# Kernel tuning notes

Hardware: AMD Instinct MI355X
Metric: run time of the kernel (lower is better)

## Reference

```python
import jax, jax.numpy as jnp
import numpy as np

DIM = 1024
HEADS = 16
HEAD_DIM = DIM // HEADS


def apply_rope(x):
    # x: (B, S, H, D)
    B, S, H, D = x.shape
    half = D // 2
    freqs = 1.0 / (10000.0 ** (jnp.arange(half, dtype=jnp.float32) / half))
    pos = jnp.arange(S, dtype=jnp.float32)
    angles = pos[:, None] * freqs[None, :]          # (S, half)
    sin = jnp.sin(angles)[None, :, None, :]
    cos = jnp.cos(angles)[None, :, None, :]
    x1, x2 = x[..., :half], x[..., half:]
    return jnp.concatenate([x1 * cos - x2 * sin, x1 * sin + x2 * cos], axis=-1)


def setup_inputs() -> dict:
    key = jax.random.key(0)
    ks = jax.random.split(key, 5)
    x = jax.random.normal(ks[0], (2, 2048, DIM), dtype=jnp.float32)
    s = 1.0 / np.sqrt(DIM)
    qkv_w = jax.random.uniform(ks[1], (3 * DIM, DIM), minval=-s, maxval=s, dtype=jnp.float32)
    qkv_b = jax.random.uniform(ks[2], (3 * DIM,), minval=-s, maxval=s, dtype=jnp.float32)
    proj_w = jax.random.uniform(ks[3], (DIM, DIM), minval=-s, maxval=s, dtype=jnp.float32)
    proj_b = jax.random.uniform(ks[4], (DIM,), minval=-s, maxval=s, dtype=jnp.float32)
    return {"x": x, "qkv_w": qkv_w, "qkv_b": qkv_b, "proj_w": proj_w, "proj_b": proj_b}


def reference(x, qkv_w, qkv_b, proj_w, proj_b):
    B, S, D = x.shape
    qkv = x @ qkv_w.T + qkv_b                       # (B, S, 3D)
    q, k, v = jnp.split(qkv, 3, axis=-1)
    q = q.reshape(B, S, HEADS, HEAD_DIM)
    k = k.reshape(B, S, HEADS, HEAD_DIM)
    v = v.reshape(B, S, HEADS, HEAD_DIM)
    q = apply_rope(q)
    k = apply_rope(k)
    scale = 1.0 / np.sqrt(HEAD_DIM)
    attn = jnp.einsum('bqhd,bkhd->bhqk', q, k) * scale
    mask = jnp.triu(jnp.ones((S, S), dtype=bool), k=1)
    attn = jnp.where(mask[None, None], -1e9, attn)
    attn = jax.nn.softmax(attn, axis=-1)
    out = jnp.einsum('bhqk,bkhd->bqhd', attn, v).reshape(B, S, D)
    return out @ proj_w.T + proj_b
```

## Files before the change

kernel.cpp:

```cpp
#include <hip/hip_runtime.h>
#include <hip/hip_bf16.h>
#include <stdint.h>

typedef unsigned short u16;
typedef __attribute__((ext_vector_type(8))) short bf16x8;
typedef __attribute__((ext_vector_type(4))) float f32x4;
typedef __attribute__((ext_vector_type(16))) float f32x16;

typedef __attribute__((address_space(1))) const void gas_t;
typedef __attribute__((address_space(3))) void las_t;

#define DEV __device__ __forceinline__

DEV float bf2f(u16 v){ union{uint32_t u; float f;} x; x.u = ((uint32_t)v)<<16; return x.f; }
DEV u16 f2bf(float f){ union{float f; uint32_t u;} x; x.f=f; uint32_t r = x.u + 0x7fff + ((x.u>>16)&1u); return (u16)(r>>16); }

DEV uint32_t pk2(float a, float b){
  return (uint32_t)f2bf(a) | ((uint32_t)f2bf(b)<<16);
}

DEV uint32_t cvtpk(float a, float b){
  uint32_t r;
  asm("v_cvt_pk_bf16_f32 %0, %1, %2" : "=v"(r) : "v"(a), "v"(b));
  return r;
}

DEV void xswap(uint32_t a, uint32_t b, int hi, uint32_t& ra, uint32_t& rb){
#if __has_builtin(__builtin_amdgcn_permlane32_swap)
  auto r = __builtin_amdgcn_permlane32_swap((int)a, (int)b, false, false);
  ra = (uint32_t)r[0]; rb = (uint32_t)r[1];
#else
  uint32_t sa = (uint32_t)__shfl_xor((int)a, 32);
  uint32_t sb = (uint32_t)__shfl_xor((int)b, 32);
  ra = hi ? sb : a;
  rb = hi ? b  : sa;
#endif
}

DEV void gload_lds16(const u16* g, u16* l){
  __builtin_amdgcn_global_load_lds((gas_t*)g, (las_t*)l, 16, 0, 0);
}

__global__ void cvt_f32_bf16(const float* __restrict__ src, u16* __restrict__ dst, int n4){
  int i = blockIdx.x*blockDim.x + threadIdx.x;
  if(i < n4){
    float4 v = ((const float4*)src)[i];
    ushort4 o; o.x=f2bf(v.x); o.y=f2bf(v.y); o.z=f2bf(v.z); o.w=f2bf(v.w);
    ((ushort4*)dst)[i] = o;
  }
}

template<int OUT_F32>
__global__ __launch_bounds__(256,3)
void gemm_bt(const u16* __restrict__ A, const u16* __restrict__ Bw,
             const float* __restrict__ bias, void* __restrict__ Cp, int N)
{
  constexpr int BK = 32, KSTEPS = 1024/BK;
  __shared__ __align__(16) u16 As[3][128][BK];
  __shared__ __align__(16) u16 Bs[3][128][BK];
  const int tid = threadIdx.x, w = tid>>6, l = tid&63;
  const int a = l&15, g = l>>4;
  const int m0 = blockIdx.y*128, n0 = blockIdx.x*128;
  const int wr = w>>1, wc = w&1;
  f32x4 zero = {0.f,0.f,0.f,0.f};
  f32x4 acc[4][4];
  #pragma unroll
  for(int m=0;m<4;m++) for(int n=0;n<4;n++) acc[m][n]=zero;

  const int srow = l>>2, scol = (l&3)*8;
  const u16* Ag = A  + (size_t)(m0 + w*32 + srow)*1024 + scol;
  const u16* Bg = Bw + (size_t)(n0 + w*32 + srow)*1024 + scol;

#define STAGE(KIDX, BUF) {                                        \
    u16* ab = &As[BUF][w*32][0];                                  \
    u16* bb = &Bs[BUF][w*32][0];                                  \
    gload_lds16(Ag + (KIDX)*BK,           ab);                    \
    gload_lds16(Ag + (KIDX)*BK + 16*1024, ab + 16*BK);            \
    gload_lds16(Bg + (KIDX)*BK,           bb);                    \
    gload_lds16(Bg + (KIDX)*BK + 16*1024, bb + 16*BK);            \
  }

  STAGE(0, 0);
  STAGE(1, 1);

  int bc = 0, bn = 2;
  for(int kt=0; kt<KSTEPS; ++kt){
    if(kt+1 < KSTEPS) asm volatile("s_waitcnt vmcnt(4)" ::: "memory");
    else              asm volatile("s_waitcnt vmcnt(0)" ::: "memory");
    __builtin_amdgcn_s_barrier();
    __builtin_amdgcn_sched_barrier(0);

    if(kt+2 < KSTEPS) STAGE(kt+2, bn);

    const u16* AsB = &As[bc][0][0];
    const u16* BsB = &Bs[bc][0][0];
    bf16x8 af[4], bf[4];
    #pragma unroll
    for(int m=0;m<4;m++) af[m] = *(const bf16x8*)(AsB + (wr*64 + m*16 + a)*BK + g*8);
    #pragma unroll
    for(int n=0;n<4;n++) bf[n] = *(const bf16x8*)(BsB + (wc*64 + n*16 + a)*BK + g*8);
    #pragma unroll
    for(int m=0;m<4;m++)
      #pragma unroll
      for(int n=0;n<4;n++)
        acc[m][n] = __builtin_amdgcn_mfma_f32_16x16x32_bf16(af[m], bf[n], acc[m][n], 0,0,0);

    bc = (bc==2) ? 0 : bc+1;
    bn = (bn==2) ? 0 : bn+1;
  }
#undef STAGE

  #pragma unroll
  for(int n=0;n<4;n++){
    int col = n0 + wc*64 + n*16 + a;
    float bv = bias[col];
    #pragma unroll
    for(int m=0;m<4;m++){
      int row = m0 + wr*64 + m*16 + g*4;
      #pragma unroll
      for(int r=0;r<4;r++){
        float v = acc[m][n][r] + bv;
        if(OUT_F32) ((float*)Cp)[(size_t)(row+r)*N + col] = v;
        else        ((u16*)Cp)[(size_t)(row+r)*N + col] = f2bf(v);
      }
    }
  }
}

__global__ void rope_relayout(const u16* __restrict__ qkv, u16* __restrict__ q_r,
                              u16* __restrict__ k_r)
{
  int t = blockIdx.x*256 + threadIdx.x;
  int gI = t&3, h=(t>>2)&15, row=t>>6;
  int s = row & 2047, b = row >> 11;
  int d0 = gI*8;
  const float QSC = 0.18033688011112042f;
  const u16* base = qkv + (size_t)row*3072 + h*64 + d0;
  union U { uint4 v; u16 e[8]; };
  U q1,q2,k1,k2, oq1,oq2,ok1,ok2;
  q1.v = *(const uint4*)(base);
  q2.v = *(const uint4*)(base+32);
  k1.v = *(const uint4*)(base+1024);
  k2.v = *(const uint4*)(base+1024+32);
  #pragma unroll
  for(int j=0;j<8;j++){
    float d = (float)(d0+j);
    float fr = __expf(-0.28782313662425574f * d);
    float ang = (float)s * fr;
    float sn, cs; sincosf(ang, &sn, &cs);
    float snq = sn*QSC, csq = cs*QSC;
    float x1 = bf2f(q1.e[j]), x2 = bf2f(q2.e[j]);
    oq1.e[j] = f2bf(x1*csq - x2*snq); oq2.e[j] = f2bf(x1*snq + x2*csq);
    x1 = bf2f(k1.e[j]); x2 = bf2f(k2.e[j]);
    ok1.e[j] = f2bf(x1*cs - x2*sn); ok2.e[j] = f2bf(x1*sn + x2*cs);
  }
  size_t o = ((size_t)(b*16+h)*2048 + s)*64 + d0;
  *(uint4*)(q_r+o) = oq1.v; *(uint4*)(q_r+o+32) = oq2.v;
  *(uint4*)(k_r+o) = ok1.v; *(uint4*)(k_r+o+32) = ok2.v;
}

__global__ __launch_bounds__(256,2)
void v_transpose(const u16* __restrict__ qkv, u16* __restrict__ vt)
{
  __shared__ uint32_t L[64*65];
  const int tid = threadIdx.x;
  const int bh = blockIdx.x & 31;
  const int stile = blockIdx.x >> 5;
  const int b = bh >> 4, h = bh & 15;
  const int s0 = stile*128;
  const int cg = tid & 7, sr = tid >> 3;
  const u16* src = qkv + (size_t)(b*2048 + s0)*3072 + 2048 + h*64 + cg*8;
  #pragma unroll
  for(int p=0;p<2;p++){
    int srow = p*64 + sr*2;
    union{uint4 v; u16 e[8];} v0, v1;
    v0.v = *(const uint4*)(src + (size_t)srow*3072);
    v1.v = *(const uint4*)(src + (size_t)(srow+1)*3072);
    #pragma unroll
    for(int jj=0;jj<8;jj++)
      L[(cg*8+jj)*65 + p*32 + sr] = (uint32_t)v0.e[jj] | ((uint32_t)v1.e[jj]<<16);
  }
  __syncthreads();
  const int w = tid>>6, ln = tid&63;
  u16* dst = vt + (size_t)bh*64*2048 + s0;
  #pragma unroll
  for(int dd=0;dd<16;dd++){
    int d = w*16 + dd;
    *(uint32_t*)(dst + (size_t)d*2048 + ln*2) = L[d*65 + ln];
  }
}

__global__ __launch_bounds__(256,4)
void attn_fwd8(const u16* __restrict__ Q, const u16* __restrict__ K,
               const u16* __restrict__ VT, u16* __restrict__ O)
{
  __shared__ __align__(16) u16 Ks[2][64][64];
  __shared__ __align__(16) u16 Vs[2][64][64];
  const int tid = threadIdx.x, w = tid>>6, ln = tid&63;
  const int lo = ln&31, hi = ln>>5;
  const int wq = w>>1, wk = w&1;
  const int b0 = blockIdx.x;
  const int bh = b0 & 31;
  const int j64 = 31 - (b0 >> 5);
  const int q0 = j64*64 + wq*32;
  const int nt = j64 + 1;

  const u16* Qb = Q  + ((size_t)bh*2048 + q0)*64;
  const u16* Kb = K  + (size_t)bh*2048*64;
  const u16* Vt = VT + (size_t)bh*64*2048;

  bf16x8 qf[4];
  #pragma unroll
  for(int s=0;s<4;s++) qf[s] = *(const bf16x8*)(Qb + lo*64 + s*16 + hi*8);

  const int rsub = ln>>3;
  const int coloff = ((ln&7) ^ rsub) * 8;
  const int wrow = (w&1)*32;
  const size_t rstride = (w<2) ? 64 : 2048;
  const u16* src0 = (w<2) ? (Kb + (size_t)(wrow+rsub)*64 + coloff)
                          : (Vt + (size_t)(wrow+rsub)*2048 + coloff);
  u16* ldsw = (w<2) ? (&Ks[0][0][0] + wrow*64) : (&Vs[0][0][0] + wrow*64);

  f32x16 oacc0, oacc1, z16;
  #pragma unroll
  for(int r=0;r<16;r++){ oacc0[r]=0.f; oacc1[r]=0.f; z16[r]=0.f; }
  float l_loc = 0.f;
  const int swz = (lo&7)<<4;

  #pragma unroll
  for(int g=0;g<4;g++) gload_lds16(src0 + (size_t)g*8*rstride, ldsw + g*512);
  __syncthreads();

  int buf = 0;
  for(int t=0; t<nt; ++t){
    if(t+1 < nt){
      const size_t koff = (w<2) ? (size_t)(t+1)*64*64 : (size_t)(t+1)*64;
      u16* dst = ldsw + (buf^1)*4096;
      #pragma unroll
      for(int g=0;g<4;g++) gload_lds16(src0 + koff + (size_t)g*8*rstride, dst + g*512);
    }

    const int kv32 = t*64 + wk*32;
    if(kv32 <= q0 + 31){
      const u16* KsB = &Ks[buf][0][0];
      const u16* VsB = &Vs[buf][0][0];
      bf16x8 kf[4], vf[4];
      #pragma unroll
      for(int s=0;s<4;s++)
        kf[s] = *(const bf16x8*)(KsB + (wk*32+lo)*64 + (((s*32 + hi*16) ^ swz)>>1));
      #pragma unroll
      for(int dt=0;dt<2;dt++)
        #pragma unroll
        for(int s2=0;s2<2;s2++)
          vf[dt*2+s2] = *(const bf16x8*)(VsB + (dt*32+lo)*64 + (((wk*64 + s2*32 + hi*16) ^ swz)>>1));

      f32x16 st = __builtin_amdgcn_mfma_f32_32x32x16_bf16(kf[0], qf[0], z16, 0,0,0);
      #pragma unroll
      for(int s=1;s<4;s++)
        st = __builtin_amdgcn_mfma_f32_32x32x16_bf16(kf[s], qf[s], st, 0,0,0);

      float p[16];
      #pragma unroll
      for(int r=0;r<16;r++) p[r] = exp2f(st[r]);
      if(kv32 == q0){
        #pragma unroll
        for(int r=0;r<16;r++){
          const int kvg = (r&3) + 8*(r>>2) + 4*hi;
          p[r] = (kvg <= lo) ? p[r] : 0.f;
        }
      }

      float sm[8];
      #pragma unroll
      for(int i=0;i<8;i++) sm[i] = p[i] + p[i+8];
      #pragma unroll
      for(int s=4;s>=1;s>>=1)
        #pragma unroll
        for(int i=0;i<s;i++) sm[i] += sm[i+s];
      l_loc += sm[0];

      uint32_t pk[8];
      #pragma unroll
      for(int i=0;i<8;i++) pk[i] = cvtpk(p[2*i], p[2*i+1]);

      union PF { bf16x8 v; uint32_t u[4]; } pf0, pf1;
      xswap(pk[0], pk[2], hi, pf0.u[0], pf0.u[2]);
      xswap(pk[1], pk[3], hi, pf0.u[1], pf0.u[3]);
      xswap(pk[4], pk[6], hi, pf1.u[0], pf1.u[2]);
      xswap(pk[5], pk[7], hi, pf1.u[1], pf1.u[3]);

      oacc0 = __builtin_amdgcn_mfma_f32_32x32x16_bf16(vf[0], pf0.v, oacc0, 0,0,0);
      oacc0 = __builtin_amdgcn_mfma_f32_32x32x16_bf16(vf[1], pf1.v, oacc0, 0,0,0);
      oacc1 = __builtin_amdgcn_mfma_f32_32x32x16_bf16(vf[2], pf0.v, oacc1, 0,0,0);
      oacc1 = __builtin_amdgcn_mfma_f32_32x32x16_bf16(vf[3], pf1.v, oacc1, 0,0,0);
    }
    __syncthreads();
    buf ^= 1;
  }

  float l_run = l_loc + __shfl_xor(l_loc, 32);

  float* LoC = (float*)&Ks[0][0][0];
  float* LlC = (float*)&Vs[0][0][0];
  if(wk == 1){
    #pragma unroll
    for(int r=0;r<16;r++){
      const int d = 4*hi + (r&3) + 8*(r>>2);
      LoC[(wq*64 + d   )*32 + lo] = oacc0[r];
      LoC[(wq*64 + d+32)*32 + lo] = oacc1[r];
    }
    if(hi==0) LlC[wq*32 + lo] = l_run;
  }
  __syncthreads();
  if(wk == 0){
    l_run += LlC[wq*32 + lo];
    #pragma unroll
    for(int r=0;r<16;r++){
      const int d = 4*hi + (r&3) + 8*(r>>2);
      oacc0[r] += LoC[(wq*64 + d   )*32 + lo];
      oacc1[r] += LoC[(wq*64 + d+32)*32 + lo];
    }
    const float invl = 1.f / l_run;
    const int row_g = (bh>>4)*2048 + q0 + lo;
    u16* Ob = O + (size_t)row_g*1024 + (bh&15)*64;
    #pragma unroll
    for(int g2=0; g2<4; g2++){
      uint2 pr;
      pr.x = pk2(oacc0[4*g2+0]*invl, oacc0[4*g2+1]*invl);
      pr.y = pk2(oacc0[4*g2+2]*invl, oacc0[4*g2+3]*invl);
      *(uint2*)(Ob + 8*g2 + 4*hi) = pr;
    }
    #pragma unroll
    for(int g2=0; g2<4; g2++){
      uint2 pr;
      pr.x = pk2(oacc1[4*g2+0]*invl, oacc1[4*g2+1]*invl);
      pr.y = pk2(oacc1[4*g2+2]*invl, oacc1[4*g2+3]*invl);
      *(uint2*)(Ob + 32 + 8*g2 + 4*hi) = pr;
    }
  }
}

extern "C" void kernel_launch(void* const* d_in, const int* in_sizes, int n_in,
                              void* d_out, int out_size, void* d_ws, size_t ws_size,
                              hipStream_t stream)
{
  const float* x      = (const float*)d_in[0];
  const float* qkv_w  = (const float*)d_in[1];
  const float* qkv_b  = (const float*)d_in[2];
  const float* proj_w = (const float*)d_in[3];
  const float* proj_b = (const float*)d_in[4];
  float* out = (float*)d_out;
  char* ws = (char*)d_ws;

  u16* xb    = (u16*)(ws);
  u16* wqkv  = (u16*)(ws + 8388608);
  u16* wproj = (u16*)(ws + 8388608 + 6291456);
  u16* qkvr  = (u16*)(ws + 16777216);
  u16* q_r   = (u16*)(ws + 41943040);
  u16* k_r   = q_r + 4194304;
  u16* vt    = k_r + 4194304;
  u16* o_b   = xb;

  cvt_f32_bf16<<<4096,256,0,stream>>>(x, xb, 1048576);
  cvt_f32_bf16<<<3072,256,0,stream>>>(qkv_w, wqkv, 786432);
  cvt_f32_bf16<<<1024,256,0,stream>>>(proj_w, wproj, 262144);

  dim3 gA(24,32);
  gemm_bt<0><<<gA,256,0,stream>>>(xb, wqkv, qkv_b, qkvr, 3072);

  rope_relayout<<<1024,256,0,stream>>>(qkvr, q_r, k_r);
  v_transpose<<<512,256,0,stream>>>(qkvr, vt);

  attn_fwd8<<<1024,256,0,stream>>>(q_r, k_r, vt, o_b);

  dim3 gC(8,32);
  gemm_bt<1><<<gC,256,0,stream>>>(o_b, wproj, proj_b, out, 1024);
}
```

Before: 120.7 us.

## Fuse rope with V transpose, pair causal tiles, triple-buffer attention KV loads

Merges the RoPE relayout and V-transpose kernels into one launch, which removes a kernel launch and an extra pass over the qkv buffer. The attention kernel now gives each block a pair of causal query tiles (p and 31-p), halving the grid and evening out per-block work. KV staging moves from double to triple buffering, with explicit vmcnt waits and a single barrier per iteration so loads run further ahead. The costs are more LDS per block, which may lower occupancy, and longer-running blocks on a 512-block grid.

```diff
diff --git a/kernel.cpp b/kernel.cpp
--- a/kernel.cpp
+++ b/kernel.cpp
@@ -127,40 +127,9 @@
   }
 }
 
-__global__ void rope_relayout(const u16* __restrict__ qkv, u16* __restrict__ q_r,
-                              u16* __restrict__ k_r)
-{
-  int t = blockIdx.x*256 + threadIdx.x;
-  int gI = t&3, h=(t>>2)&15, row=t>>6;
-  int s = row & 2047, b = row >> 11;
-  int d0 = gI*8;
-  const float QSC = 0.18033688011112042f;
-  const u16* base = qkv + (size_t)row*3072 + h*64 + d0;
-  union U { uint4 v; u16 e[8]; };
-  U q1,q2,k1,k2, oq1,oq2,ok1,ok2;
-  q1.v = *(const uint4*)(base);
-  q2.v = *(const uint4*)(base+32);
-  k1.v = *(const uint4*)(base+1024);
-  k2.v = *(const uint4*)(base+1024+32);
-  #pragma unroll
-  for(int j=0;j<8;j++){
-    float d = (float)(d0+j);
-    float fr = __expf(-0.28782313662425574f * d);
-    float ang = (float)s * fr;
-    float sn, cs; sincosf(ang, &sn, &cs);
-    float snq = sn*QSC, csq = cs*QSC;
-    float x1 = bf2f(q1.e[j]), x2 = bf2f(q2.e[j]);
-    oq1.e[j] = f2bf(x1*csq - x2*snq); oq2.e[j] = f2bf(x1*snq + x2*csq);
-    x1 = bf2f(k1.e[j]); x2 = bf2f(k2.e[j]);
-    ok1.e[j] = f2bf(x1*cs - x2*sn); ok2.e[j] = f2bf(x1*sn + x2*cs);
-  }
-  size_t o = ((size_t)(b*16+h)*2048 + s)*64 + d0;
-  *(uint4*)(q_r+o) = oq1.v; *(uint4*)(q_r+o+32) = oq2.v;
-  *(uint4*)(k_r+o) = ok1.v; *(uint4*)(k_r+o+32) = ok2.v;
-}
-
 __global__ __launch_bounds__(256,2)
-void v_transpose(const u16* __restrict__ qkv, u16* __restrict__ vt)
+void rope_vt(const u16* __restrict__ qkv, u16* __restrict__ q_r,
+             u16* __restrict__ k_r, u16* __restrict__ vt)
 {
   __shared__ uint32_t L[64*65];
   const int tid = threadIdx.x;
@@ -168,50 +137,78 @@
   const int stile = blockIdx.x >> 5;
   const int b = bh >> 4, h = bh & 15;
   const int s0 = stile*128;
+
   const int cg = tid & 7, sr = tid >> 3;
-  const u16* src = qkv + (size_t)(b*2048 + s0)*3072 + 2048 + h*64 + cg*8;
-  #pragma unroll
-  for(int p=0;p<2;p++){
-    int srow = p*64 + sr*2;
-    union{uint4 v; u16 e[8];} v0, v1;
-    v0.v = *(const uint4*)(src + (size_t)srow*3072);
-    v1.v = *(const uint4*)(src + (size_t)(srow+1)*3072);
-    #pragma unroll
-    for(int jj=0;jj<8;jj++)
-      L[(cg*8+jj)*65 + p*32 + sr] = (uint32_t)v0.e[jj] | ((uint32_t)v1.e[jj]<<16);
+  const u16* vsrc = qkv + (size_t)(b*2048 + s0)*3072 + 2048 + h*64 + cg*8;
+  union U4 { uint4 v; u16 e[8]; };
+  U4 v0a, v1a, v0b, v1b;
+  v0a.v = *(const uint4*)(vsrc + (size_t)(sr*2    )*3072);
+  v1a.v = *(const uint4*)(vsrc + (size_t)(sr*2 + 1)*3072);
+  v0b.v = *(const uint4*)(vsrc + (size_t)(64 + sr*2    )*3072);
+  v1b.v = *(const uint4*)(vsrc + (size_t)(64 + sr*2 + 1)*3072);
+  #pragma unroll
+  for(int jj=0;jj<8;jj++){
+    L[(cg*8+jj)*65 + sr]      = (uint32_t)v0a.e[jj] | ((uint32_t)v1a.e[jj]<<16);
+    L[(cg*8+jj)*65 + 32 + sr] = (uint32_t)v0b.e[jj] | ((uint32_t)v1b.e[jj]<<16);
   }
   __syncthreads();
-  const int w = tid>>6, ln = tid&63;
-  u16* dst = vt + (size_t)bh*64*2048 + s0;
-  #pragma unroll
-  for(int dd=0;dd<16;dd++){
-    int d = w*16 + dd;
-    *(uint32_t*)(dst + (size_t)d*2048 + ln*2) = L[d*65 + ln];
+  {
+    const int w = tid>>6, ln = tid&63;
+    u16* dst = vt + (size_t)bh*64*2048 + s0;
+    #pragma unroll
+    for(int dd=0;dd<16;dd++){
+      int d = w*16 + dd;
+      *(uint32_t*)(dst + (size_t)d*2048 + ln*2) = L[d*65 + ln];
+    }
+  }
+
+  const float QSC = 0.18033688011112042f;
+  #pragma unroll
+  for(int it=0; it<2; ++it){
+    int t2 = it*256 + tid;
+    int row = t2>>2, gI = t2&3;
+    int s = s0 + row;
+    int d0 = gI*8;
+    const u16* base = qkv + (size_t)(b*2048 + s)*3072 + h*64 + d0;
+    union U { uint4 v; u16 e[8]; };
+    U q1,q2,k1,k2, oq1,oq2,ok1,ok2;
+    q1.v = *(const uint4*)(base);
+    q2.v = *(const uint4*)(base+32);
+    k1.v = *(const uint4*)(base+1024);
+    k2.v = *(const uint4*)(base+1024+32);
+    #pragma unroll
+    for(int j=0;j<8;j++){
+      float d = (float)(d0+j);
+      float fr = __expf(-0.28782313662425574f * d);
+      float ang = (float)s * fr;
+      float sn, cs; sincosf(ang, &sn, &cs);
+      float snq = sn*QSC, csq = cs*QSC;
+      float x1 = bf2f(q1.e[j]), x2 = bf2f(q2.e[j]);
+      oq1.e[j] = f2bf(x1*csq - x2*snq); oq2.e[j] = f2bf(x1*snq + x2*csq);
+      x1 = bf2f(k1.e[j]); x2 = bf2f(k2.e[j]);
+      ok1.e[j] = f2bf(x1*cs - x2*sn); ok2.e[j] = f2bf(x1*sn + x2*cs);
+    }
+    size_t o = ((size_t)bh*2048 + s)*64 + d0;
+    *(uint4*)(q_r+o) = oq1.v; *(uint4*)(q_r+o+32) = oq2.v;
+    *(uint4*)(k_r+o) = ok1.v; *(uint4*)(k_r+o+32) = ok2.v;
   }
 }
 
 __global__ __launch_bounds__(256,4)
-void attn_fwd8(const u16* __restrict__ Q, const u16* __restrict__ K,
+void attn_fwd9(const u16* __restrict__ Q, const u16* __restrict__ K,
                const u16* __restrict__ VT, u16* __restrict__ O)
 {
-  __shared__ __align__(16) u16 Ks[2][64][64];
-  __shared__ __align__(16) u16 Vs[2][64][64];
+  __shared__ __align__(16) u16 Ks[3][64][64];
+  __shared__ __align__(16) u16 Vs[3][64][64];
   const int tid = threadIdx.x, w = tid>>6, ln = tid&63;
   const int lo = ln&31, hi = ln>>5;
   const int wq = w>>1, wk = w&1;
   const int b0 = blockIdx.x;
   const int bh = b0 & 31;
-  const int j64 = 31 - (b0 >> 5);
-  const int q0 = j64*64 + wq*32;
-  const int nt = j64 + 1;
-
-  const u16* Qb = Q  + ((size_t)bh*2048 + q0)*64;
+  const int p  = b0 >> 5;
+
   const u16* Kb = K  + (size_t)bh*2048*64;
   const u16* Vt = VT + (size_t)bh*64*2048;
-
-  bf16x8 qf[4];
-  #pragma unroll
-  for(int s=0;s<4;s++) qf[s] = *(const bf16x8*)(Qb + lo*64 + s*16 + hi*8);
 
   const int rsub = ln>>3;
   const int coloff = ((ln&7) ^ rsub) * 8;
@@ -221,121 +218,144 @@
                           : (Vt + (size_t)(wrow+rsub)*2048 + coloff);
   u16* ldsw = (w<2) ? (&Ks[0][0][0] + wrow*64) : (&Vs[0][0][0] + wrow*64);
 
-  f32x16 oacc0, oacc1, z16;
-  #pragma unroll
-  for(int r=0;r<16;r++){ oacc0[r]=0.f; oacc1[r]=0.f; z16[r]=0.f; }
-  float l_loc = 0.f;
   const int swz = (lo&7)<<4;
-
-  #pragma unroll
-  for(int g=0;g<4;g++) gload_lds16(src0 + (size_t)g*8*rstride, ldsw + g*512);
-  __syncthreads();
-
-  int buf = 0;
-  for(int t=0; t<nt; ++t){
-    if(t+1 < nt){
-      const size_t koff = (w<2) ? (size_t)(t+1)*64*64 : (size_t)(t+1)*64;
-      u16* dst = ldsw + (buf^1)*4096;
-      #pragma unroll
-      for(int g=0;g<4;g++) gload_lds16(src0 + koff + (size_t)g*8*rstride, dst + g*512);
-    }
-
-    const int kv32 = t*64 + wk*32;
-    if(kv32 <= q0 + 31){
-      const u16* KsB = &Ks[buf][0][0];
-      const u16* VsB = &Vs[buf][0][0];
-      bf16x8 kf[4], vf[4];
-      #pragma unroll
-      for(int s=0;s<4;s++)
-        kf[s] = *(const bf16x8*)(KsB + (wk*32+lo)*64 + (((s*32 + hi*16) ^ swz)>>1));
-      #pragma unroll
-      for(int dt=0;dt<2;dt++)
-        #pragma unroll
-        for(int s2=0;s2<2;s2++)
-          vf[dt*2+s2] = *(const bf16x8*)(VsB + (dt*32+lo)*64 + (((wk*64 + s2*32 + hi*16) ^ swz)>>1));
-
-      f32x16 st = __builtin_amdgcn_mfma_f32_32x32x16_bf16(kf[0], qf[0], z16, 0,0,0);
-      #pragma unroll
-      for(int s=1;s<4;s++)
-        st = __builtin_amdgcn_mfma_f32_32x32x16_bf16(kf[s], qf[s], st, 0,0,0);
-
-      float p[16];
-      #pragma unroll
-      for(int r=0;r<16;r++) p[r] = exp2f(st[r]);
-      if(kv32 == q0){
-        #pragma unroll
-        for(int r=0;r<16;r++){
-          const int kvg = (r&3) + 8*(r>>2) + 4*hi;
-          p[r] = (kvg <= lo) ? p[r] : 0.f;
+  f32x16 z16;
+  #pragma unroll
+  for(int r=0;r<16;r++) z16[r]=0.f;
+
+  #pragma unroll 1
+  for(int ph=0; ph<2; ++ph){
+    const int j64 = ph ? (31-p) : p;
+    const int q0 = j64*64 + wq*32;
+    const int nt = j64 + 1;
+    const u16* Qb = Q + ((size_t)bh*2048 + q0)*64;
+    bf16x8 qf[4];
+    #pragma unroll
+    for(int s=0;s<4;s++) qf[s] = *(const bf16x8*)(Qb + lo*64 + s*16 + hi*8);
+    f32x16 oacc0 = z16, oacc1 = z16;
+    float l_loc = 0.f;
+
+    __syncthreads();
+    #pragma unroll
+    for(int g=0;g<4;g++) gload_lds16(src0 + (size_t)g*8*rstride, ldsw + g*512);
+    {
+      const size_t koff1 = (w<2) ? (size_t)64*64 : (size_t)64;
+      #pragma unroll
+      for(int g=0;g<4;g++) gload_lds16(src0 + koff1 + (size_t)g*8*rstride, ldsw + 4096 + g*512);
+    }
+
+    int bc = 0, bn = 2;
+    for(int t=0; t<nt; ++t){
+      if(t+1 < nt) asm volatile("s_waitcnt vmcnt(4)" ::: "memory");
+      else         asm volatile("s_waitcnt vmcnt(0)" ::: "memory");
+      __builtin_amdgcn_s_barrier();
+      __builtin_amdgcn_sched_barrier(0);
+
+      if(t+2 < nt){
+        const size_t koff = (w<2) ? (size_t)(t+2)*64*64 : (size_t)(t+2)*64;
+        u16* dst = ldsw + bn*4096;
+        #pragma unroll
+        for(int g=0;g<4;g++) gload_lds16(src0 + koff + (size_t)g*8*rstride, dst + g*512);
+      }
+
+      const int kv32 = t*64 + wk*32;
+      if(kv32 <= q0 + 31){
+        const u16* KsB = &Ks[bc][0][0];
+        const u16* VsB = &Vs[bc][0][0];
+        bf16x8 kf[4], vf[4];
+        #pragma unroll
+        for(int s=0;s<4;s++)
+          kf[s] = *(const bf16x8*)(KsB + (wk*32+lo)*64 + (((s*32 + hi*16) ^ swz)>>1));
+        #pragma unroll
+        for(int dt=0;dt<2;dt++)
+          #pragma unroll
+          for(int s2=0;s2<2;s2++)
+            vf[dt*2+s2] = *(const bf16x8*)(VsB + (dt*32+lo)*64 + (((wk*64 + s2*32 + hi*16) ^ swz)>>1));
+
+        f32x16 st = __builtin_amdgcn_mfma_f32_32x32x16_bf16(kf[0], qf[0], z16, 0,0,0);
+        #pragma unroll
+        for(int s=1;s<4;s++)
+          st = __builtin_amdgcn_mfma_f32_32x32x16_bf16(kf[s], qf[s], st, 0,0,0);
+
+        float pp[16];
+        #pragma unroll
+        for(int r=0;r<16;r++) pp[r] = exp2f(st[r]);
+        if(kv32 == q0){
+          #pragma unroll
+          for(int r=0;r<16;r++){
+            const int kvg = (r&3) + 8*(r>>2) + 4*hi;
+            pp[r] = (kvg <= lo) ? pp[r] : 0.f;
+          }
         }
-      }
-
-      float sm[8];
-      #pragma unroll
-      for(int i=0;i<8;i++) sm[i] = p[i] + p[i+8];
-      #pragma unroll
-      for(int s=4;s>=1;s>>=1)
-        #pragma unroll
-        for(int i=0;i<s;i++) sm[i] += sm[i+s];
-      l_loc += sm[0];
-
-      uint32_t pk[8];
-      #pragma unroll
-      for(int i=0;i<8;i++) pk[i] = cvtpk(p[2*i], p[2*i+1]);
-
-      union PF { bf16x8 v; uint32_t u[4]; } pf0, pf1;
-      xswap(pk[0], pk[2], hi, pf0.u[0], pf0.u[2]);
-      xswap(pk[1], pk[3], hi, pf0.u[1], pf0.u[3]);
-      xswap(pk[4], pk[6], hi, pf1.u[0], pf1.u[2]);
-      xswap(pk[5], pk[7], hi, pf1.u[1], pf1.u[3]);
-
-      oacc0 = __builtin_amdgcn_mfma_f32_32x32x16_bf16(vf[0], pf0.v, oacc0, 0,0,0);
-      oacc0 = __builtin_amdgcn_mfma_f32_32x32x16_bf16(vf[1], pf1.v, oacc0, 0,0,0);
-      oacc1 = __builtin_amdgcn_mfma_f32_32x32x16_bf16(vf[2], pf0.v, oacc1, 0,0,0);
-      oacc1 = __builtin_amdgcn_mfma_f32_32x32x16_bf16(vf[3], pf1.v, oacc1, 0,0,0);
+
+        float sm[8];
+        #pragma unroll
+        for(int i=0;i<8;i++) sm[i] = pp[i] + pp[i+8];
+        #pragma unroll
+        for(int s=4;s>=1;s>>=1)
+          #pragma unroll
+          for(int i=0;i<s;i++) sm[i] += sm[i+s];
+        l_loc += sm[0];
+
+        uint32_t pk[8];
+        #pragma unroll
+        for(int i=0;i<8;i++) pk[i] = cvtpk(pp[2*i], pp[2*i+1]);
+
+        union PF { bf16x8 v; uint32_t u[4]; } pf0, pf1;
+        xswap(pk[0], pk[2], hi, pf0.u[0], pf0.u[2]);
+        xswap(pk[1], pk[3], hi, pf0.u[1], pf0.u[3]);
+        xswap(pk[4], pk[6], hi, pf1.u[0], pf1.u[2]);
+        xswap(pk[5], pk[7], hi, pf1.u[1], pf1.u[3]);
+
+        oacc0 = __builtin_amdgcn_mfma_f32_32x32x16_bf16(vf[0], pf0.v, oacc0, 0,0,0);
+        oacc0 = __builtin_amdgcn_mfma_f32_32x32x16_bf16(vf[1], pf1.v, oacc0, 0,0,0);
+        oacc1 = __builtin_amdgcn_mfma_f32_32x32x16_bf16(vf[2], pf0.v, oacc1, 0,0,0);
+        oacc1 = __builtin_amdgcn_mfma_f32_32x32x16_bf16(vf[3], pf1.v, oacc1, 0,0,0);
+      }
+      bc = (bc==2) ? 0 : bc+1;
+      bn = (bn==2) ? 0 : bn+1;
     }
     __syncthreads();
-    buf ^= 1;
-  }
-
-  float l_run = l_loc + __shfl_xor(l_loc, 32);
-
-  float* LoC = (float*)&Ks[0][0][0];
-  float* LlC = (float*)&Vs[0][0][0];
-  if(wk == 1){
-    #pragma unroll
-    for(int r=0;r<16;r++){
-      const int d = 4*hi + (r&3) + 8*(r>>2);
-      LoC[(wq*64 + d   )*32 + lo] = oacc0[r];
-      LoC[(wq*64 + d+32)*32 + lo] = oacc1[r];
-    }
-    if(hi==0) LlC[wq*32 + lo] = l_run;
-  }
-  __syncthreads();
-  if(wk == 0){
-    l_run += LlC[wq*32 + lo];
-    #pragma unroll
-    for(int r=0;r<16;r++){
-      const int d = 4*hi + (r&3) + 8*(r>>2);
-      oacc0[r] += LoC[(wq*64 + d   )*32 + lo];
-      oacc1[r] += LoC[(wq*64 + d+32)*32 + lo];
-    }
-    const float invl = 1.f / l_run;
-    const int row_g = (bh>>4)*2048 + q0 + lo;
-    u16* Ob = O + (size_t)row_g*1024 + (bh&15)*64;
-    #pragma unroll
-    for(int g2=0; g2<4; g2++){
-      uint2 pr;
-      pr.x = pk2(oacc0[4*g2+0]*invl, oacc0[4*g2+1]*invl);
-      pr.y = pk2(oacc0[4*g2+2]*invl, oacc0[4*g2+3]*invl);
-      *(uint2*)(Ob + 8*g2 + 4*hi) = pr;
-    }
-    #pragma unroll
-    for(int g2=0; g2<4; g2++){
-      uint2 pr;
-      pr.x = pk2(oacc1[4*g2+0]*invl, oacc1[4*g2+1]*invl);
-      pr.y = pk2(oacc1[4*g2+2]*invl, oacc1[4*g2+3]*invl);
-      *(uint2*)(Ob + 32 + 8*g2 + 4*hi) = pr;
+
+    float l_run = l_loc + __shfl_xor(l_loc, 32);
+
+    float* LoC = (float*)&Ks[0][0][0];
+    float* LlC = (float*)&Vs[0][0][0];
+    if(wk == 1){
+      #pragma unroll
+      for(int r=0;r<16;r++){
+        const int d = 4*hi + (r&3) + 8*(r>>2);
+        LoC[(wq*64 + d   )*32 + lo] = oacc0[r];
+        LoC[(wq*64 + d+32)*32 + lo] = oacc1[r];
+      }
+      if(hi==0) LlC[wq*32 + lo] = l_run;
+    }
+    __syncthreads();
+    if(wk == 0){
+      l_run += LlC[wq*32 + lo];
+      #pragma unroll
+      for(int r=0;r<16;r++){
+        const int d = 4*hi + (r&3) + 8*(r>>2);
+        oacc0[r] += LoC[(wq*64 + d   )*32 + lo];
+        oacc1[r] += LoC[(wq*64 + d+32)*32 + lo];
+      }
+      const float invl = 1.f / l_run;
+      const int row_g = (bh>>4)*2048 + q0 + lo;
+      u16* Ob = O + (size_t)row_g*1024 + (bh&15)*64;
+      #pragma unroll
+      for(int g2=0; g2<4; g2++){
+        uint2 pr;
+        pr.x = pk2(oacc0[4*g2+0]*invl, oacc0[4*g2+1]*invl);
+        pr.y = pk2(oacc0[4*g2+2]*invl, oacc0[4*g2+3]*invl);
+        *(uint2*)(Ob + 8*g2 + 4*hi) = pr;
+      }
+      #pragma unroll
+      for(int g2=0; g2<4; g2++){
+        uint2 pr;
+        pr.x = pk2(oacc1[4*g2+0]*invl, oacc1[4*g2+1]*invl);
+        pr.y = pk2(oacc1[4*g2+2]*invl, oacc1[4*g2+3]*invl);
+        *(uint2*)(Ob + 32 + 8*g2 + 4*hi) = pr;
+      }
     }
   }
 }
@@ -368,10 +388,9 @@
   dim3 gA(24,32);
   gemm_bt<0><<<gA,256,0,stream>>>(xb, wqkv, qkv_b, qkvr, 3072);
 
-  rope_relayout<<<1024,256,0,stream>>>(qkvr, q_r, k_r);
-  v_transpose<<<512,256,0,stream>>>(qkvr, vt);
-
-  attn_fwd8<<<1024,256,0,stream>>>(q_r, k_r, vt, o_b);
+  rope_vt<<<512,256,0,stream>>>(qkvr, q_r, k_r, vt);
+
+  attn_fwd9<<<512,256,0,stream>>>(q_r, k_r, vt, o_b);
 
   dim3 gC(8,32);
   gemm_bt<1><<<gC,256,0,stream>>>(o_b, wproj, proj_b, out, 1024);
```

After: 127.2 us. +5.4%, slower.
